# Performance work log

Measured on AMD Instinct MI355X. Metric: run time of the kernel, lower is better.

Reference implementation:

```python
import jax, jax.numpy as jnp
import numpy as np

NUM_DEM = 2
VOCAB = 10000
EMB = 128


def setup_inputs() -> dict:
    key = jax.random.key(0)
    k_src, k_emb, k_w1, k_w2 = jax.random.split(key, 4)
    B = 16384
    # 0/1 multi-hot style input (demographic cols also 0/1; math identical)
    src = jax.random.randint(k_src, (B, NUM_DEM + VOCAB), 0, 2).astype(jnp.float32)
    embed = jax.random.normal(k_emb, (VOCAB, EMB), dtype=jnp.float32)
    W1 = jax.random.normal(k_w1, (NUM_DEM + EMB, 16), dtype=jnp.float32) * 0.1
    b1 = jnp.full((16,), 0.01, dtype=jnp.float32)
    W2 = jax.random.normal(k_w2, (16, 2), dtype=jnp.float32) * 0.1
    b2 = jnp.full((2,), 0.01, dtype=jnp.float32)
    return {"src": src, "embed": embed, "W1": W1, "b1": b1, "W2": W2, "b2": b2}


def reference(src, embed, W1, b1, W2, b2):
    dem = src[:, :NUM_DEM]                         # [B, 2]
    codes = src[:, NUM_DEM:].astype(jnp.int32)     # [B, V]
    mask = (codes != 0).astype(embed.dtype)        # multi-hot indicator [B, V]
    counts = jnp.sum(mask, axis=1, keepdims=True)  # [B, 1]
    # fused multi-hot gather + mean pooling (embedding-bag mean)
    pooled = (mask @ embed) / counts               # [B, EMB]
    x = jnp.concatenate([dem, pooled], axis=1)     # [B, 2+EMB]
    h = jnp.tanh(x @ W1 + b1)
    return h @ W2 + b2                             # [B, 2]
```

## Files before the change

### kernel.cpp

```cpp
#include <hip/hip_runtime.h>

#define NUM_DEM 2
#define VOCAB 10000
#define EMB 128
#define NROWS 16384
#define ROWLEN (NUM_DEM + VOCAB)
#define KSTEPS 313
#define PCOLS 132
#define BPACK_USHORTS (KSTEPS * 4096)
#define BPACK_BYTES (BPACK_USHORTS * 2)

typedef float f32x4 __attribute__((ext_vector_type(4)));
typedef __bf16 bf16x8 __attribute__((ext_vector_type(8)));
typedef short s16x8 __attribute__((ext_vector_type(8)));

union Frag {
    s16x8 s;
    bf16x8 b;
    unsigned int u[4];
    unsigned short h[8];
};

__device__ __forceinline__ unsigned short f2bf_rtne(float f) {
    unsigned int u = __float_as_uint(f);
    u += 0x7FFFu + ((u >> 16) & 1u);
    return (unsigned short)(u >> 16);
}

__global__ void pack_embed_k(const float* __restrict__ embed,
                             unsigned short* __restrict__ bp) {
    int id = blockIdx.x * blockDim.x + threadIdx.x;
    if (id >= KSTEPS * 8 * 64) return;
    int l = id & 63;
    int c = (id >> 6) & 7;
    int t = id >> 9;
    int kbase = t * 32 + ((l >> 4) * 8);
    int n = c * 16 + (l & 15);
    unsigned short v[8];
#pragma unroll
    for (int j = 0; j < 8; ++j) {
        int k = kbase + j;
        float f = (k < VOCAB) ? embed[(size_t)k * EMB + n] : 0.0f;
        v[j] = f2bf_rtne(f);
    }
    uint4 w;
    w.x = (unsigned int)v[0] | ((unsigned int)v[1] << 16);
    w.y = (unsigned int)v[2] | ((unsigned int)v[3] << 16);
    w.z = (unsigned int)v[4] | ((unsigned int)v[5] << 16);
    w.w = (unsigned int)v[6] | ((unsigned int)v[7] << 16);
    *reinterpret_cast<uint4*>(bp + (size_t)id * 8) = w;
}

typedef const __attribute__((address_space(1))) unsigned int* gas_u32p;
typedef __attribute__((address_space(3))) unsigned int* las_u32p;
#define GLOAD_LDS16(g, l)                                                              \
    __builtin_amdgcn_global_load_lds((gas_u32p)(g), (las_u32p)(l), 16, 0, 0)

__global__ __launch_bounds__(256, 4) void main_gemm_k(
    const float* __restrict__ src, const unsigned short* __restrict__ bp,
    float* __restrict__ part, int nch) {
    __shared__ alignas(16) unsigned short ldsB[4096];

    const int tid = threadIdx.x;
    const int lane = tid & 63;
    const int wid = tid >> 6;
    const int rb = blockIdx.x & 255;
    const int ch = blockIdx.x >> 8;
    const int t0 = (KSTEPS * ch) / nch;
    const int t1 = (KSTEPS * (ch + 1)) / nch;

    const int rowbase = rb * 64 + wid * 16;
    const int arow = rowbase + (lane & 15);
    const int kgrp8 = (lane >> 4) * 8;
    const float* asrc = src + (size_t)arow * ROWLEN + NUM_DEM + kgrp8;

    f32x4 pacc[8];
#pragma unroll
    for (int f = 0; f < 8; ++f) pacc[f] = (f32x4){0.f, 0.f, 0.f, 0.f};
    f32x4 cacc = (f32x4){0.f, 0.f, 0.f, 0.f};

    Frag onesf;
    {
        unsigned short o = ((lane & 15) == 0) ? (unsigned short)0x3F80 : (unsigned short)0;
        unsigned int ow = (unsigned int)o | ((unsigned int)o << 16);
        onesf.u[0] = ow; onesf.u[1] = ow; onesf.u[2] = ow; onesf.u[3] = ow;
    }

    for (int t = t0; t < t1; ++t) {
        const unsigned short* gB = bp + (size_t)t * 4096;
        GLOAD_LDS16(gB + wid * 1024 + lane * 8, ldsB + wid * 1024 + lane * 8);
        GLOAD_LDS16(gB + wid * 1024 + 512 + lane * 8, ldsB + wid * 1024 + 512 + lane * 8);

        float4 a0, a1;
        int kb = t * 32 + kgrp8;
        if (kb + 8 <= VOCAB) {
            const float* ap = asrc + (size_t)t * 32;
            a0 = *reinterpret_cast<const float4*>(ap);
            a1 = *reinterpret_cast<const float4*>(ap + 4);
        } else {
            a0 = make_float4(0.f, 0.f, 0.f, 0.f);
            a1 = a0;
        }

        __syncthreads();

        Frag af;
        af.u[0] = __builtin_amdgcn_perm(__float_as_uint(a0.y), __float_as_uint(a0.x), 0x07060302u);
        af.u[1] = __builtin_amdgcn_perm(__float_as_uint(a0.w), __float_as_uint(a0.z), 0x07060302u);
        af.u[2] = __builtin_amdgcn_perm(__float_as_uint(a1.y), __float_as_uint(a1.x), 0x07060302u);
        af.u[3] = __builtin_amdgcn_perm(__float_as_uint(a1.w), __float_as_uint(a1.z), 0x07060302u);

#pragma unroll
        for (int f = 0; f < 8; ++f) {
            Frag bfr;
            bfr.s = *reinterpret_cast<const s16x8*>(ldsB + f * 512 + lane * 8);
            pacc[f] = __builtin_amdgcn_mfma_f32_16x16x32_bf16(af.b, bfr.b, pacc[f], 0, 0, 0);
        }
        cacc = __builtin_amdgcn_mfma_f32_16x16x32_bf16(af.b, onesf.b, cacc, 0, 0, 0);

        __syncthreads();
    }

    const int rlo = (lane >> 4) * 4;
    float* pch = part + (size_t)ch * NROWS * PCOLS;
#pragma unroll
    for (int f = 0; f < 8; ++f) {
#pragma unroll
        for (int r = 0; r < 4; ++r) {
            int row = rowbase + rlo + r;
            pch[(size_t)row * PCOLS + f * 16 + (lane & 15)] = pacc[f][r];
        }
    }
    if ((lane & 15) == 0) {
#pragma unroll
        for (int r = 0; r < 4; ++r) {
            int row = rowbase + rlo + r;
            pch[(size_t)row * PCOLS + 128] = cacc[r];
        }
    }
}

__global__ __launch_bounds__(256) void mlp_k(const float* __restrict__ part,
                                             const float* __restrict__ src,
                                             const float* __restrict__ W1,
                                             const float* __restrict__ b1,
                                             const float* __restrict__ W2,
                                             const float* __restrict__ b2,
                                             float* __restrict__ out, int nch) {
    __shared__ float xls[16][131];
    __shared__ float hls[16][16];
    __shared__ float cnt[16];
    const int tid = threadIdx.x;
    const int rb = blockIdx.x * 16;

    if (tid < 16) {
        float s = 0.f;
        for (int c = 0; c < nch; ++c)
            s += part[((size_t)c * NROWS + rb + tid) * PCOLS + 128];
        cnt[tid] = s;
    }
    if (tid >= 16 && tid < 48) {
        int r = (tid - 16) >> 1, d = (tid - 16) & 1;
        xls[r][d] = src[(size_t)(rb + r) * ROWLEN + d];
    }
    __syncthreads();

    for (int idx = tid; idx < 16 * 128; idx += 256) {
        int r = idx >> 7, col = idx & 127;
        float s = 0.f;
        for (int c = 0; c < nch; ++c)
            s += part[((size_t)c * NROWS + rb + r) * PCOLS + col];
        xls[r][NUM_DEM + col] = s / cnt[r];
    }
    __syncthreads();

    {
        int r = tid >> 4, u = tid & 15;
        float acc = b1[u];
        for (int i = 0; i < NUM_DEM + EMB; ++i) acc += xls[r][i] * W1[i * 16 + u];
        hls[r][u] = tanhf(acc);
    }
    __syncthreads();

    if (tid < 32) {
        int r = tid >> 1, o = tid & 1;
        float acc = b2[o];
#pragma unroll
        for (int u = 0; u < 16; ++u) acc += hls[r][u] * W2[u * 2 + o];
        out[(size_t)(rb + r) * 2 + o] = acc;
    }
}

extern "C" void kernel_launch(void* const* d_in, const int* in_sizes, int n_in,
                              void* d_out, int out_size, void* d_ws, size_t ws_size,
                              hipStream_t stream) {
    const float* src = (const float*)d_in[0];
    const float* embed = (const float*)d_in[1];
    const float* W1 = (const float*)d_in[2];
    const float* b1 = (const float*)d_in[3];
    const float* W2 = (const float*)d_in[4];
    const float* b2 = (const float*)d_in[5];
    float* out = (float*)d_out;

    unsigned short* bpack = (unsigned short*)d_ws;
    float* part = (float*)((char*)d_ws + BPACK_BYTES);

    const size_t part1 = (size_t)NROWS * PCOLS * sizeof(float);
    int nch = 4;
    while (nch > 1 && BPACK_BYTES + part1 * (size_t)nch > ws_size) nch >>= 1;

    hipLaunchKernelGGL(pack_embed_k, dim3((KSTEPS * 8 * 64 + 255) / 256), dim3(256), 0,
                       stream, embed, bpack);
    hipLaunchKernelGGL(main_gemm_k, dim3(256 * nch), dim3(256), 0, stream, src, bpack,
                       part, nch);
    hipLaunchKernelGGL(mlp_k, dim3(NROWS / 16), dim3(256), 0, stream, part, src, W1, b1,
                       W2, b2, out, nch);
}
```

Measured before the change: 209.9 us.

## Load B fragments directly from global, prefetch A, drop LDS barriers

The main GEMM kernel stops staging the packed embedding tile in LDS through global_load_lds. Each wave now reads its B fragments straight from global memory, where every wave in the block re-reads the same small L2-resident tile. A loads are software-prefetched one step ahead with nontemporal loads so the streamed src bypasses cache retention. Removing both __syncthreads per K step eliminates barrier stalls, at the cost of four times more B traffic through L1/L2 and more registers for eight B fragments plus the prefetched A.

```diff
diff --git a/kernel.cpp b/kernel.cpp
--- a/kernel.cpp
+++ b/kernel.cpp
@@ -51,16 +51,9 @@
     *reinterpret_cast<uint4*>(bp + (size_t)id * 8) = w;
 }
 
-typedef const __attribute__((address_space(1))) unsigned int* gas_u32p;
-typedef __attribute__((address_space(3))) unsigned int* las_u32p;
-#define GLOAD_LDS16(g, l)                                                              \
-    __builtin_amdgcn_global_load_lds((gas_u32p)(g), (las_u32p)(l), 16, 0, 0)
-
 __global__ __launch_bounds__(256, 4) void main_gemm_k(
     const float* __restrict__ src, const unsigned short* __restrict__ bp,
     float* __restrict__ part, int nch) {
-    __shared__ alignas(16) unsigned short ldsB[4096];
-
     const int tid = threadIdx.x;
     const int lane = tid & 63;
     const int wid = tid >> 6;
@@ -86,23 +79,29 @@
         onesf.u[0] = ow; onesf.u[1] = ow; onesf.u[2] = ow; onesf.u[3] = ow;
     }
 
+    const s16x8* blane = reinterpret_cast<const s16x8*>(bp + (size_t)t0 * 4096 + lane * 8);
+
+    f32x4 a0n = (f32x4){0.f, 0.f, 0.f, 0.f}, a1n = a0n;
+    if (t0 * 32 + kgrp8 + 8 <= VOCAB) {
+        const float* ap = asrc + (size_t)t0 * 32;
+        a0n = __builtin_nontemporal_load(reinterpret_cast<const f32x4*>(ap));
+        a1n = __builtin_nontemporal_load(reinterpret_cast<const f32x4*>(ap + 4));
+    }
+
     for (int t = t0; t < t1; ++t) {
-        const unsigned short* gB = bp + (size_t)t * 4096;
-        GLOAD_LDS16(gB + wid * 1024 + lane * 8, ldsB + wid * 1024 + lane * 8);
-        GLOAD_LDS16(gB + wid * 1024 + 512 + lane * 8, ldsB + wid * 1024 + 512 + lane * 8);
-
-        float4 a0, a1;
-        int kb = t * 32 + kgrp8;
-        if (kb + 8 <= VOCAB) {
-            const float* ap = asrc + (size_t)t * 32;
-            a0 = *reinterpret_cast<const float4*>(ap);
-            a1 = *reinterpret_cast<const float4*>(ap + 4);
-        } else {
-            a0 = make_float4(0.f, 0.f, 0.f, 0.f);
-            a1 = a0;
+        f32x4 a0 = a0n, a1 = a1n;
+        a0n = (f32x4){0.f, 0.f, 0.f, 0.f};
+        a1n = a0n;
+        if (t + 1 < t1 && (t + 1) * 32 + kgrp8 + 8 <= VOCAB) {
+            const float* ap = asrc + (size_t)(t + 1) * 32;
+            a0n = __builtin_nontemporal_load(reinterpret_cast<const f32x4*>(ap));
+            a1n = __builtin_nontemporal_load(reinterpret_cast<const f32x4*>(ap + 4));
         }
 
-        __syncthreads();
+        Frag bfr[8];
+#pragma unroll
+        for (int f = 0; f < 8; ++f) bfr[f].s = blane[f * 64];
+        blane += 512;
 
         Frag af;
         af.u[0] = __builtin_amdgcn_perm(__float_as_uint(a0.y), __float_as_uint(a0.x), 0x07060302u);
@@ -111,14 +110,9 @@
         af.u[3] = __builtin_amdgcn_perm(__float_as_uint(a1.w), __float_as_uint(a1.z), 0x07060302u);
 
 #pragma unroll
-        for (int f = 0; f < 8; ++f) {
-            Frag bfr;
-            bfr.s = *reinterpret_cast<const s16x8*>(ldsB + f * 512 + lane * 8);
-            pacc[f] = __builtin_amdgcn_mfma_f32_16x16x32_bf16(af.b, bfr.b, pacc[f], 0, 0, 0);
-        }
+        for (int f = 0; f < 8; ++f)
+            pacc[f] = __builtin_amdgcn_mfma_f32_16x16x32_bf16(af.b, bfr[f].b, pacc[f], 0, 0, 0);
         cacc = __builtin_amdgcn_mfma_f32_16x16x32_bf16(af.b, onesf.b, cacc, 0, 0, 0);
-
-        __syncthreads();
     }
 
     const int rlo = (lane >> 4) * 4;
```

Result: slower. 347.2 us (+65.4%).

## Software-pipeline main GEMM with triple-buffered LDS and register prefetch of A

Applied to the files above, without the earlier changes.

Restructures the main GEMM loop into a 3-stage software pipeline. B tiles go into a triple-buffered LDS region, and A fragments are prefetched two steps ahead into rotating registers with nontemporal loads. The two __syncthreads per step are replaced by a single barrier behind a manual vmcnt wait. The goal is to hide global load latency behind the MFMA work. The cost is more LDS and registers, so launch bounds drop from 4 to 3 blocks per SM.

```diff
diff --git a/kernel.cpp b/kernel.cpp
--- a/kernel.cpp
+++ b/kernel.cpp
@@ -56,10 +56,56 @@
 #define GLOAD_LDS16(g, l)                                                              \
     __builtin_amdgcn_global_load_lds((gas_u32p)(g), (las_u32p)(l), 16, 0, 0)
 
-__global__ __launch_bounds__(256, 4) void main_gemm_k(
+#define PIPE_BODY(T, JC, JI, BR, BW)                                                   \
+    {                                                                                  \
+        const int t_ = (T);                                                            \
+        const int tst_ = (t_ + 1 < t1) ? (t_ + 1) : (t1 - 1);                          \
+        const unsigned short* gB_ = bp + (size_t)tst_ * 4096 + wid * 1024 + lane * 8;  \
+        unsigned short* lB_ = ldsB + (BW)*4096 + wid * 1024 + lane * 8;                \
+        GLOAD_LDS16(gB_, lB_);                                                         \
+        GLOAD_LDS16(gB_ + 512, lB_ + 512);                                             \
+        asm volatile("" ::: "memory");                                                 \
+        {                                                                              \
+            int tld_ = (t_ + 2 < t1) ? (t_ + 2) : (t1 - 1);                            \
+            int kbA_ = tld_ * 32 + kgrp8;                                              \
+            const f32x4* ap_ = reinterpret_cast<const f32x4*>(                         \
+                asrc + ((kbA_ + 8 <= VOCAB) ? (size_t)tld_ * 32 : (size_t)0));         \
+            aS##JI##0 = __builtin_nontemporal_load(ap_);                               \
+            aS##JI##1 = __builtin_nontemporal_load(ap_ + 1);                           \
+        }                                                                              \
+        asm volatile("s_waitcnt vmcnt(6)" ::: "memory");                               \
+        __builtin_amdgcn_s_barrier();                                                  \
+        {                                                                              \
+            int kb_ = t_ * 32 + kgrp8;                                                 \
+            bool vA_ = (kb_ + 8 <= VOCAB);                                             \
+            f32x4 za_ = (f32x4){0.f, 0.f, 0.f, 0.f};                                   \
+            f32x4 a0_ = vA_ ? aS##JC##0 : za_;                                         \
+            f32x4 a1_ = vA_ ? aS##JC##1 : za_;                                         \
+            Frag af_;                                                                  \
+            af_.u[0] = __builtin_amdgcn_perm(__float_as_uint(a0_.y),                   \
+                                             __float_as_uint(a0_.x), 0x07060302u);     \
+            af_.u[1] = __builtin_amdgcn_perm(__float_as_uint(a0_.w),                   \
+                                             __float_as_uint(a0_.z), 0x07060302u);     \
+            af_.u[2] = __builtin_amdgcn_perm(__float_as_uint(a1_.y),                   \
+                                             __float_as_uint(a1_.x), 0x07060302u);     \
+            af_.u[3] = __builtin_amdgcn_perm(__float_as_uint(a1_.w),                   \
+                                             __float_as_uint(a1_.z), 0x07060302u);     \
+            const unsigned short* rB_ = ldsB + (BR)*4096 + lane * 8;                   \
+            _Pragma("unroll") for (int f = 0; f < 8; ++f) {                            \
+                Frag bfr_;                                                             \
+                bfr_.s = *reinterpret_cast<const s16x8*>(rB_ + f * 512);               \
+                pacc[f] = __builtin_amdgcn_mfma_f32_16x16x32_bf16(af_.b, bfr_.b,       \
+                                                                  pacc[f], 0, 0, 0);   \
+            }                                                                          \
+            cacc = __builtin_amdgcn_mfma_f32_16x16x32_bf16(af_.b, onesf.b, cacc, 0, 0, \
+                                                           0);                         \
+        }                                                                              \
+    }
+
+__global__ __launch_bounds__(256, 3) void main_gemm_k(
     const float* __restrict__ src, const unsigned short* __restrict__ bp,
     float* __restrict__ part, int nch) {
-    __shared__ alignas(16) unsigned short ldsB[4096];
+    __shared__ alignas(16) unsigned short ldsB[3 * 4096];
 
     const int tid = threadIdx.x;
     const int lane = tid & 63;
@@ -86,39 +132,40 @@
         onesf.u[0] = ow; onesf.u[1] = ow; onesf.u[2] = ow; onesf.u[3] = ow;
     }
 
-    for (int t = t0; t < t1; ++t) {
-        const unsigned short* gB = bp + (size_t)t * 4096;
-        GLOAD_LDS16(gB + wid * 1024 + lane * 8, ldsB + wid * 1024 + lane * 8);
-        GLOAD_LDS16(gB + wid * 1024 + 512 + lane * 8, ldsB + wid * 1024 + 512 + lane * 8);
-
-        float4 a0, a1;
-        int kb = t * 32 + kgrp8;
-        if (kb + 8 <= VOCAB) {
-            const float* ap = asrc + (size_t)t * 32;
-            a0 = *reinterpret_cast<const float4*>(ap);
-            a1 = *reinterpret_cast<const float4*>(ap + 4);
-        } else {
-            a0 = make_float4(0.f, 0.f, 0.f, 0.f);
-            a1 = a0;
-        }
-
-        __syncthreads();
-
-        Frag af;
-        af.u[0] = __builtin_amdgcn_perm(__float_as_uint(a0.y), __float_as_uint(a0.x), 0x07060302u);
-        af.u[1] = __builtin_amdgcn_perm(__float_as_uint(a0.w), __float_as_uint(a0.z), 0x07060302u);
-        af.u[2] = __builtin_amdgcn_perm(__float_as_uint(a1.y), __float_as_uint(a1.x), 0x07060302u);
-        af.u[3] = __builtin_amdgcn_perm(__float_as_uint(a1.w), __float_as_uint(a1.z), 0x07060302u);
-
-#pragma unroll
-        for (int f = 0; f < 8; ++f) {
-            Frag bfr;
-            bfr.s = *reinterpret_cast<const s16x8*>(ldsB + f * 512 + lane * 8);
-            pacc[f] = __builtin_amdgcn_mfma_f32_16x16x32_bf16(af.b, bfr.b, pacc[f], 0, 0, 0);
-        }
-        cacc = __builtin_amdgcn_mfma_f32_16x16x32_bf16(af.b, onesf.b, cacc, 0, 0, 0);
-
-        __syncthreads();
+    f32x4 aS00, aS01, aS10, aS11, aS20, aS21;
+
+    {
+        const unsigned short* gB_ = bp + (size_t)t0 * 4096 + wid * 1024 + lane * 8;
+        unsigned short* lB_ = ldsB + wid * 1024 + lane * 8;
+        GLOAD_LDS16(gB_, lB_);
+        GLOAD_LDS16(gB_ + 512, lB_ + 512);
+        asm volatile("" ::: "memory");
+        {
+            int kbA_ = t0 * 32 + kgrp8;
+            const f32x4* ap_ = reinterpret_cast<const f32x4*>(
+                asrc + ((kbA_ + 8 <= VOCAB) ? (size_t)t0 * 32 : (size_t)0));
+            aS00 = __builtin_nontemporal_load(ap_);
+            aS01 = __builtin_nontemporal_load(ap_ + 1);
+        }
+        asm volatile("" ::: "memory");
+        {
+            int t_ = t0 + 1;
+            int kbA_ = t_ * 32 + kgrp8;
+            const f32x4* ap_ = reinterpret_cast<const f32x4*>(
+                asrc + ((kbA_ + 8 <= VOCAB) ? (size_t)t_ * 32 : (size_t)0));
+            aS10 = __builtin_nontemporal_load(ap_);
+            aS11 = __builtin_nontemporal_load(ap_ + 1);
+        }
+    }
+
+    int t = t0;
+    for (; t + 3 <= t1; t += 3) {
+        PIPE_BODY(t, 0, 2, 0, 1);
+        PIPE_BODY(t + 1, 1, 0, 1, 2);
+        PIPE_BODY(t + 2, 2, 1, 2, 0);
+    }
+    if (t < t1) {
+        PIPE_BODY(t, 0, 2, 0, 1);
     }
 
     const int rlo = (lane >> 4) * 4;
```

Measured after the change: 295.3 us. +40.7%, slower.
